# Kernel tuning notes

Hardware: AMD Instinct MI355X
Metric: run time of the kernel (lower is better)

Reference implementation:

```python
import jax, jax.numpy as jnp
import numpy as np

H = 16
D_MODEL = 1024
D_K = D_MODEL // H
SEQ = 2048
BATCH = 2


def setup_inputs() -> dict:
    key = jax.random.key(0)
    ks = jax.random.split(key, 11)
    s = 1.0 / np.sqrt(D_MODEL)
    inp = {
        "query": jax.random.normal(ks[0], (SEQ, BATCH, D_MODEL), jnp.float32),
        "key_": jax.random.normal(ks[1], (SEQ, BATCH, D_MODEL), jnp.float32),
        "value": jax.random.normal(ks[2], (SEQ, BATCH, D_MODEL), jnp.float32),
        "Wq": jax.random.uniform(ks[3], (D_MODEL, D_MODEL), jnp.float32, -s, s),
        "bq": jax.random.uniform(ks[4], (D_MODEL,), jnp.float32, -s, s),
        "Wk": jax.random.uniform(ks[5], (D_MODEL, D_MODEL), jnp.float32, -s, s),
        "bk": jax.random.uniform(ks[6], (D_MODEL,), jnp.float32, -s, s),
        "Wv": jax.random.uniform(ks[7], (D_MODEL, D_MODEL), jnp.float32, -s, s),
        "bv": jax.random.uniform(ks[8], (D_MODEL,), jnp.float32, -s, s),
        "Wo": jax.random.uniform(ks[9], (D_MODEL, D_MODEL), jnp.float32, -s, s),
        "bo": jax.random.uniform(ks[10], (D_MODEL,), jnp.float32, -s, s),
    }
    return inp


def _mha(query, key_, value, Wq, bq, Wk, bk, Wv, bv, Wo, bo):
    S, B, D = query.shape
    # torch Linear: x @ W.T + b; then view(S,B,h,dk).transpose(0,2) -> [h,B,S,dk]
    def proj(x, W, b):
        return jnp.transpose((x @ W.T + b).reshape(S, B, H, D_K), (2, 1, 0, 3))

    q = proj(query, Wq, bq)   # [h, b, S, dk]
    k = proj(key_, Wk, bk)
    v = proj(value, Wv, bv)

    scores = jnp.einsum("hbqd,hbkd->hbqk", q, k) / jnp.sqrt(
        jnp.asarray(D_K, q.dtype)
    )  # [h, b, S, S]
    p_attn = jax.nn.softmax(scores, axis=-1)  # dropout p=0.0 -> identity
    x = jnp.einsum("hbqk,hbkd->hbqd", p_attn, v)  # [h, b, S, dk]
    x = jnp.transpose(x, (2, 1, 0, 3)).reshape(S, B, D)  # back to [S, B, D]
    return x @ Wo.T + bo


def reference(query, key_, value, Wq, bq, Wk, bk, Wv, bv, Wo, bo):
    return _mha(query, key_, value, Wq, bq, Wk, bk, Wv, bv, Wo, bo)
```

## Files before the change

kernel.cpp:

```cpp
#include <hip/hip_runtime.h>

#define SEQ   2048
#define BATCH 2
#define DM    1024
#define NH    16
#define DKD   64
#define MROWS (SEQ*BATCH)

#define QSCALE 0.18033688011112042f

using bf16x8 = __attribute__((ext_vector_type(8))) __bf16;
using bf16x4 = __attribute__((ext_vector_type(4))) __bf16;
using bf16x2 = __attribute__((ext_vector_type(2))) __bf16;
using f32x4  = __attribute__((ext_vector_type(4))) float;
using f32x16 = __attribute__((ext_vector_type(16))) float;

__device__ __forceinline__ void gld_lds16(const __bf16* g, __bf16* l) {
  __builtin_amdgcn_global_load_lds(
      (__attribute__((address_space(1))) void*)(g),
      (__attribute__((address_space(3))) void*)(l), 16, 0, 0);
}

__global__ __launch_bounds__(256) void cvt_all(
    const float* __restrict__ s0, const float* __restrict__ s1,
    const float* __restrict__ s2, const float* __restrict__ s3,
    const float* __restrict__ s4, const float* __restrict__ s5,
    const float* __restrict__ s6,
    __bf16* __restrict__ d0, __bf16* __restrict__ d1, __bf16* __restrict__ d2,
    __bf16* __restrict__ d3, __bf16* __restrict__ d4, __bf16* __restrict__ d5,
    __bf16* __restrict__ d6, int n_big, int n_small) {
  int y = blockIdx.y;
  const float* s; __bf16* d;
  switch (y) {
    case 0: s = s0; d = d0; break;
    case 1: s = s1; d = d1; break;
    case 2: s = s2; d = d2; break;
    case 3: s = s3; d = d3; break;
    case 4: s = s4; d = d4; break;
    case 5: s = s5; d = d5; break;
    default: s = s6; d = d6; break;
  }
  int n = (y < 3) ? n_big : n_small;
  int i = (blockIdx.x * 256 + threadIdx.x) * 8;
  if (i >= n) return;
  const float4* sp = (const float4*)(s + i);
  float4 a = sp[0], b = sp[1];
  bf16x8 v;
  v[0]=(__bf16)a.x; v[1]=(__bf16)a.y; v[2]=(__bf16)a.z; v[3]=(__bf16)a.w;
  v[4]=(__bf16)b.x; v[5]=(__bf16)b.y; v[6]=(__bf16)b.z; v[7]=(__bf16)b.w;
  *(bf16x8*)(d + i) = v;
}

__device__ __forceinline__ void gemm_core(const __bf16* __restrict__ A,
                                          const __bf16* __restrict__ Bt,
                                          __bf16* Ash, __bf16* Bsh,
                                          f32x4 acc[4][4], int m0, int n0) {
  const int K = DM;
  int tid = threadIdx.x;
  int lane = tid & 63, quad = lane >> 4, l16 = lane & 15, sw = l16 & 7;
  int w = tid >> 6;
  int wm = (w & 1) * 64, wn = (w >> 1) * 64;
  for (int k0 = 0; k0 < K; k0 += 64) {
    __syncthreads();
#pragma unroll
    for (int it = 0; it < 4; ++it) {
      int c   = tid + it * 256;
      int row = c >> 3, pp = c & 7;
      int ko  = (pp ^ (row & 7)) << 3;
      int base = (tid - lane + it * 256) * 8;
      gld_lds16(A  + (size_t)(m0 + row) * K + k0 + ko, Ash + base);
      gld_lds16(Bt + (size_t)(n0 + row) * K + k0 + ko, Bsh + base);
    }
    __syncthreads();
#pragma unroll
    for (int kk = 0; kk < 2; ++kk) {
      bf16x8 af[4], bfr[4];
#pragma unroll
      for (int mi = 0; mi < 4; mi++)
        af[mi] = *(const bf16x8*)&Ash[(wm + mi * 16 + l16) * 64 +
                                      (((kk * 4 + quad) ^ sw) << 3)];
#pragma unroll
      for (int ni = 0; ni < 4; ni++)
        bfr[ni] = *(const bf16x8*)&Bsh[(wn + ni * 16 + l16) * 64 +
                                       (((kk * 4 + quad) ^ sw) << 3)];
#pragma unroll
      for (int mi = 0; mi < 4; mi++)
#pragma unroll
        for (int ni = 0; ni < 4; ni++)
          acc[mi][ni] = __builtin_amdgcn_mfma_f32_16x16x32_bf16(
              af[mi], bfr[ni], acc[mi][ni], 0, 0, 0);
    }
  }
}

__global__ __launch_bounds__(256, 3) void gemm_qkv(
    const __bf16* __restrict__ Xq, const __bf16* __restrict__ Xk,
    const __bf16* __restrict__ Xv, const __bf16* __restrict__ Wqkv,
    const float* __restrict__ bqp, const float* __restrict__ bkp,
    const float* __restrict__ bvp,
    __bf16* __restrict__ Qb, __bf16* __restrict__ Kb, __bf16* __restrict__ Vt) {
  __shared__ __bf16 Ash[128 * 64], Bsh[128 * 64];
  __shared__ __bf16 Esh[4][16 * 72];
  int z = blockIdx.z;
  const __bf16* A   = (z == 0) ? Xq : (z == 1) ? Xk : Xv;
  const __bf16* Bt  = Wqkv + (size_t)z * (DM * DM);
  const float* bias = (z == 0) ? bqp : (z == 1) ? bkp : bvp;
  int m0 = blockIdx.y * 128, n0 = blockIdx.x * 128;
  f32x4 acc[4][4] = {};
  gemm_core(A, Bt, Ash, Bsh, acc, m0, n0);

  int tid = threadIdx.x, lane = tid & 63, quad = lane >> 4, l16 = lane & 15;
  int w = tid >> 6, wm = (w & 1) * 64, wn = (w >> 1) * 64;
  __bf16* E = Esh[w];
  int n_base = n0 + wn;
  int hh = n_base >> 6;
  float scale = (z == 0) ? QSCALE : 1.0f;
  float bb[4];
#pragma unroll
  for (int ni = 0; ni < 4; ni++) bb[ni] = bias[n_base + ni * 16 + l16] * scale;

  if (z == 2) {
#pragma unroll
    for (int ni = 0; ni < 4; ni++) {
#pragma unroll
      for (int mi = 0; mi < 4; mi++) {
        int s0 = mi * 8 + quad * 2;
        bf16x2 p0, p1;
        p0[0] = (__bf16)(acc[mi][ni][0] + bb[ni]);
        p0[1] = (__bf16)(acc[mi][ni][2] + bb[ni]);
        p1[0] = (__bf16)(acc[mi][ni][1] + bb[ni]);
        p1[1] = (__bf16)(acc[mi][ni][3] + bb[ni]);
        *(bf16x2*)&E[l16 * 72 + s0]      = p0;
        *(bf16x2*)&E[l16 * 72 + 32 + s0] = p1;
      }
      asm volatile("s_waitcnt lgkmcnt(0)" ::: "memory");
#pragma unroll
      for (int pass = 0; pass < 2; pass++) {
        int ddl = pass * 8 + (lane >> 3);
        int col = (lane & 7) * 8;
        bf16x8 v = *(const bf16x8*)&E[ddl * 72 + col];
        int b2 = col >> 5, sl = col & 31;
        int dd = ni * 16 + ddl;
        int sg = ((m0 + wm) >> 1) + sl;
        *(bf16x8*)&Vt[(((size_t)hh * BATCH + b2) * DKD + dd) * SEQ + sg] = v;
      }
      asm volatile("s_waitcnt lgkmcnt(0)" ::: "memory");
    }
  } else {
    __bf16* Out = (z == 0) ? Qb : Kb;
#pragma unroll
    for (int mi = 0; mi < 4; mi++) {
#pragma unroll
      for (int ni = 0; ni < 4; ni++)
#pragma unroll
        for (int r = 0; r < 4; r++)
          E[(quad * 4 + r) * 72 + ni * 16 + l16] =
              (__bf16)fmaf(acc[mi][ni][r], scale, bb[ni]);
      asm volatile("s_waitcnt lgkmcnt(0)" ::: "memory");
#pragma unroll
      for (int pass = 0; pass < 2; pass++) {
        int row16 = pass * 8 + (lane >> 3);
        int coll  = (lane & 7) * 8;
        bf16x8 v = *(const bf16x8*)&E[row16 * 72 + coll];
        int m = m0 + wm + mi * 16 + row16;
        int s = m >> 1, b2 = m & 1;
        *(bf16x8*)&Out[(((size_t)hh * BATCH + b2) * SEQ + s) * DKD + coll] = v;
      }
      asm volatile("s_waitcnt lgkmcnt(0)" ::: "memory");
    }
  }
}

__global__ __launch_bounds__(256, 3) void gemm_out(
    const __bf16* __restrict__ A, const __bf16* __restrict__ Bt,
    const float* __restrict__ bias, float* __restrict__ out) {
  __shared__ __bf16 Ash[64 * 64], Bsh[128 * 64];
  const int K = DM;
  int m0 = blockIdx.y * 64, n0 = blockIdx.x * 128;
  int tid = threadIdx.x;
  int lane = tid & 63, quad = lane >> 4, l16 = lane & 15, sw = l16 & 7;
  int w = tid >> 6;
  int wm = (w & 1) * 32, wn = (w >> 1) * 64;
  f32x4 acc[2][4] = {};
  for (int k0 = 0; k0 < K; k0 += 64) {
    __syncthreads();
#pragma unroll
    for (int it = 0; it < 2; ++it) {
      int c = tid + it * 256;
      int row = c >> 3, pp = c & 7;
      int ko = (pp ^ (row & 7)) << 3;
      gld_lds16(A + (size_t)(m0 + row) * K + k0 + ko,
                Ash + (tid - lane + it * 256) * 8);
    }
#pragma unroll
    for (int it = 0; it < 4; ++it) {
      int c = tid + it * 256;
      int row = c >> 3, pp = c & 7;
      int ko = (pp ^ (row & 7)) << 3;
      gld_lds16(Bt + (size_t)(n0 + row) * K + k0 + ko,
                Bsh + (tid - lane + it * 256) * 8);
    }
    __syncthreads();
#pragma unroll
    for (int kk = 0; kk < 2; ++kk) {
      bf16x8 af[2], bfr[4];
#pragma unroll
      for (int mi = 0; mi < 2; mi++)
        af[mi] = *(const bf16x8*)&Ash[(wm + mi * 16 + l16) * 64 +
                                      (((kk * 4 + quad) ^ sw) << 3)];
#pragma unroll
      for (int ni = 0; ni < 4; ni++)
        bfr[ni] = *(const bf16x8*)&Bsh[(wn + ni * 16 + l16) * 64 +
                                       (((kk * 4 + quad) ^ sw) << 3)];
#pragma unroll
      for (int mi = 0; mi < 2; mi++)
#pragma unroll
        for (int ni = 0; ni < 4; ni++)
          acc[mi][ni] = __builtin_amdgcn_mfma_f32_16x16x32_bf16(
              af[mi], bfr[ni], acc[mi][ni], 0, 0, 0);
    }
  }
#pragma unroll
  for (int ni = 0; ni < 4; ni++) {
    int n = n0 + wn + ni * 16 + l16;
    float bb = bias[n];
#pragma unroll
    for (int mi = 0; mi < 2; mi++) {
#pragma unroll
      for (int r = 0; r < 4; r++) {
        int m = m0 + wm + mi * 16 + quad * 4 + r;
        out[(size_t)m * DM + n] = acc[mi][ni][r] + bb;
      }
    }
  }
}

__global__ __launch_bounds__(256, 2) void flash_attn(
    const __bf16* __restrict__ Qg, const __bf16* __restrict__ Kg,
    const __bf16* __restrict__ Vtg, __bf16* __restrict__ Xa) {
  __shared__ __bf16 Ksh[2][64 * 64];
  __shared__ __bf16 Vsh[2][64 * 64];
  int tid = threadIdx.x, w = tid >> 6, lane = tid & 63;
  int l32 = lane & 31, hf = lane >> 5;
  int n = blockIdx.x;
  int hb = n & 31, qi = n >> 5;
  int hd = hb >> 1, b = hb & 1, q0 = qi * 128;
  int qbase = q0 + w * 32;
  size_t hboff = ((size_t)hd * BATCH + b) * SEQ * DKD;
  const __bf16* Qp = Qg + hboff;
  const __bf16* Kp = Kg + hboff;
  const __bf16* Vp = Vtg + hboff;

  bf16x8 qf[4];
#pragma unroll
  for (int kd = 0; kd < 4; kd++)
    qf[kd] = *(const bf16x8*)(
        Qp + (size_t)(qbase + l32) * DKD + kd * 16 + hf * 8);

  f32x16 o0 = {0,0,0,0,0,0,0,0,0,0,0,0,0,0,0,0};
  f32x16 o1 = {0,0,0,0,0,0,0,0,0,0,0,0,0,0,0,0};
  float l0 = 0.f, l1 = 0.f;

#pragma unroll
  for (int it = 0; it < 2; ++it) {
    int c = tid + it * 256;
    int r = c >> 3, pp = c & 7;
    int off = (pp ^ (r & 7)) << 3;
    gld_lds16(Kp + (size_t)r * DKD + off, Ksh[0] + c * 8);
    gld_lds16(Vp + (size_t)r * SEQ + off, Vsh[0] + c * 8);
  }

  for (int t = 0; t < SEQ / 64; ++t) {
    __syncthreads();
    if (t + 1 < SEQ / 64) {
      int k0n = (t + 1) * 64, bn = (t + 1) & 1;
#pragma unroll
      for (int it = 0; it < 2; ++it) {
        int c = tid + it * 256;
        int r = c >> 3, pp = c & 7;
        int off = (pp ^ (r & 7)) << 3;
        gld_lds16(Kp + (size_t)(k0n + r) * DKD + off, Ksh[bn] + c * 8);
        gld_lds16(Vp + (size_t)r * SEQ + k0n + off, Vsh[bn] + c * 8);
      }
    }
    const __bf16* Kb_ = Ksh[t & 1];
    const __bf16* Vb_ = Vsh[t & 1];

#pragma unroll
    for (int jt = 0; jt < 2; ++jt) {
      int rk = jt * 32 + l32;
      f32x16 s = {0,0,0,0,0,0,0,0,0,0,0,0,0,0,0,0};
#pragma unroll
      for (int kd = 0; kd < 4; kd++) {
        bf16x8 kf = *(const bf16x8*)&Kb_[rk * 64 +
                                         (((kd * 2 + hf) ^ (rk & 7)) << 3)];
        s = __builtin_amdgcn_mfma_f32_32x32x16_bf16(kf, qf[kd], s, 0, 0, 0);
      }
      unsigned L[4][2];
#pragma unroll
      for (int bq = 0; bq < 4; bq++) {
        float p0 = exp2f(s[4 * bq + 0]);
        float p1 = exp2f(s[4 * bq + 1]);
        float p2 = exp2f(s[4 * bq + 2]);
        float p3 = exp2f(s[4 * bq + 3]);
        l0 += p0 + p2;
        l1 += p1 + p3;
        asm("v_cvt_pk_bf16_f32 %0, %1, %2" : "=v"(L[bq][0]) : "v"(p0), "v"(p1));
        asm("v_cvt_pk_bf16_f32 %0, %1, %2" : "=v"(L[bq][1]) : "v"(p2), "v"(p3));
      }
#pragma unroll
      for (int kp = 0; kp < 2; kp++) {
        unsigned a0 = L[2 * kp][0], b0 = L[2 * kp + 1][0];
        unsigned a1 = L[2 * kp][1], b1 = L[2 * kp + 1][1];
        asm("v_permlane32_swap_b32 %0, %1" : "+v"(a0), "+v"(b0));
        asm("v_permlane32_swap_b32 %0, %1" : "+v"(a1), "+v"(b1));
        unsigned pw[4] = {a0, a1, b0, b1};
        bf16x8 pa;
        __builtin_memcpy(&pa, pw, 16);
        int ks = jt * 2 + kp;
        {
          int rv = l32;
          bf16x8 vb = *(const bf16x8*)&Vb_[rv * 64 +
                                           (((ks * 2 + hf) ^ (rv & 7)) << 3)];
          o0 = __builtin_amdgcn_mfma_f32_32x32x16_bf16(pa, vb, o0, 0, 0, 0);
        }
        {
          int rv = 32 + l32;
          bf16x8 vb = *(const bf16x8*)&Vb_[rv * 64 +
                                           (((ks * 2 + hf) ^ (rv & 7)) << 3)];
          o1 = __builtin_amdgcn_mfma_f32_32x32x16_bf16(pa, vb, o1, 0, 0, 0);
        }
      }
    }
  }

  float l_ = l0 + l1;
  l_ += __shfl_xor(l_, 32, 64);
  float linv = 1.0f / l_;

#pragma unroll
  for (int r = 0; r < 16; ++r) {
    int qrow = (r & 3) + 8 * (r >> 2) + 4 * hf;
    float li = __shfl(linv, qrow, 64);
    int q = qbase + qrow;
    __bf16* dst = Xa + ((size_t)q * BATCH + b) * DM + hd * DKD;
    dst[l32]      = (__bf16)(o0[r] * li);
    dst[32 + l32] = (__bf16)(o1[r] * li);
  }
}

extern "C" void kernel_launch(void* const* d_in, const int* in_sizes, int n_in,
                              void* d_out, int out_size, void* d_ws,
                              size_t ws_size, hipStream_t stream) {
  (void)in_sizes; (void)n_in; (void)out_size; (void)ws_size;
  const float* query = (const float*)d_in[0];
  const float* key_  = (const float*)d_in[1];
  const float* value = (const float*)d_in[2];
  const float* Wq = (const float*)d_in[3];
  const float* bq = (const float*)d_in[4];
  const float* Wk = (const float*)d_in[5];
  const float* bk = (const float*)d_in[6];
  const float* Wv = (const float*)d_in[7];
  const float* bv = (const float*)d_in[8];
  const float* Wo = (const float*)d_in[9];
  const float* bo = (const float*)d_in[10];

  const size_t NX = (size_t)MROWS * DM;
  const size_t NW = (size_t)DM * DM;
  __bf16* p    = (__bf16*)d_ws;
  __bf16* Xq   = p; p += NX;
  __bf16* Xk   = p; p += NX;
  __bf16* Xv   = p; p += NX;
  __bf16* Wqkv = p; p += 3 * NW;
  __bf16* Wob  = p; p += NW;
  __bf16* Qb   = p; p += NX;
  __bf16* Kb   = p; p += NX;
  __bf16* Vt   = p; p += NX;
  __bf16* Xa   = Xq;

  cvt_all<<<dim3((unsigned)(NX / 2048), 7), 256, 0, stream>>>(
      query, key_, value, Wq, Wk, Wv, Wo,
      Xq, Xk, Xv, Wqkv, Wqkv + NW, Wqkv + 2 * NW, Wob, (int)NX, (int)NW);

  gemm_qkv<<<dim3(DM / 128, MROWS / 128, 3), 256, 0, stream>>>(
      Xq, Xk, Xv, Wqkv, bq, bk, bv, Qb, Kb, Vt);
  flash_attn<<<dim3(512), 256, 0, stream>>>(Qb, Kb, Vt, Xa);
  gemm_out<<<dim3(DM / 128, MROWS / 64), 256, 0, stream>>>(
      Xa, Wob, bo, (float*)d_out);
}
```

Baseline: 225.9 us.

## Split attention over key halves with fp32 partials and a combine kernel

Each attention block now processes half of the key sequence, doubling the grid to fill more compute units, and launch bounds are raised to allow more blocks per CU. Unnormalized fp32 partial outputs and row sums are written to workspace, and a new combine kernel sums them, normalizes, and converts to bf16. This relies on the fixed-scale softmax having no running max, so the partials add directly. The trade-off is extra global memory traffic for the fp32 partials and an additional kernel launch.

```diff
diff --git a/kernel.cpp b/kernel.cpp
--- a/kernel.cpp
+++ b/kernel.cpp
@@ -235,17 +235,22 @@
   }
 }
 
-__global__ __launch_bounds__(256, 2) void flash_attn(
+__global__ __launch_bounds__(256, 4) void flash_attn(
     const __bf16* __restrict__ Qg, const __bf16* __restrict__ Kg,
-    const __bf16* __restrict__ Vtg, __bf16* __restrict__ Xa) {
+    const __bf16* __restrict__ Vtg,
+    float* __restrict__ Op0, float* __restrict__ Op1,
+    float* __restrict__ Lp0, float* __restrict__ Lp1) {
   __shared__ __bf16 Ksh[2][64 * 64];
   __shared__ __bf16 Vsh[2][64 * 64];
   int tid = threadIdx.x, w = tid >> 6, lane = tid & 63;
   int l32 = lane & 31, hf = lane >> 5;
   int n = blockIdx.x;
-  int hb = n & 31, qi = n >> 5;
+  int hb = n & 31, qi = (n >> 5) & 15, jh = n >> 9;
   int hd = hb >> 1, b = hb & 1, q0 = qi * 128;
   int qbase = q0 + w * 32;
+  int t0 = jh * 16;
+  float* Op = jh ? Op1 : Op0;
+  float* Lp = jh ? Lp1 : Lp0;
   size_t hboff = ((size_t)hd * BATCH + b) * SEQ * DKD;
   const __bf16* Qp = Qg + hboff;
   const __bf16* Kp = Kg + hboff;
@@ -266,14 +271,14 @@
     int c = tid + it * 256;
     int r = c >> 3, pp = c & 7;
     int off = (pp ^ (r & 7)) << 3;
-    gld_lds16(Kp + (size_t)r * DKD + off, Ksh[0] + c * 8);
-    gld_lds16(Vp + (size_t)r * SEQ + off, Vsh[0] + c * 8);
-  }
-
-  for (int t = 0; t < SEQ / 64; ++t) {
+    gld_lds16(Kp + (size_t)(t0 * 64 + r) * DKD + off, Ksh[0] + c * 8);
+    gld_lds16(Vp + (size_t)r * SEQ + t0 * 64 + off, Vsh[0] + c * 8);
+  }
+
+  for (int tt = 0; tt < 16; ++tt) {
     __syncthreads();
-    if (t + 1 < SEQ / 64) {
-      int k0n = (t + 1) * 64, bn = (t + 1) & 1;
+    if (tt + 1 < 16) {
+      int k0n = (t0 + tt + 1) * 64, bn = (tt + 1) & 1;
 #pragma unroll
       for (int it = 0; it < 2; ++it) {
         int c = tid + it * 256;
@@ -283,8 +288,8 @@
         gld_lds16(Vp + (size_t)r * SEQ + k0n + off, Vsh[bn] + c * 8);
       }
     }
-    const __bf16* Kb_ = Ksh[t & 1];
-    const __bf16* Vb_ = Vsh[t & 1];
+    const __bf16* Kb_ = Ksh[tt & 1];
+    const __bf16* Vb_ = Vsh[tt & 1];
 
 #pragma unroll
     for (int jt = 0; jt < 2; ++jt) {
@@ -336,17 +341,41 @@
 
   float l_ = l0 + l1;
   l_ += __shfl_xor(l_, 32, 64);
-  float linv = 1.0f / l_;
+  if (hf == 0)
+    Lp[((size_t)hd * BATCH + b) * SEQ + qbase + l32] = l_;
 
 #pragma unroll
   for (int r = 0; r < 16; ++r) {
     int qrow = (r & 3) + 8 * (r >> 2) + 4 * hf;
-    float li = __shfl(linv, qrow, 64);
     int q = qbase + qrow;
-    __bf16* dst = Xa + ((size_t)q * BATCH + b) * DM + hd * DKD;
-    dst[l32]      = (__bf16)(o0[r] * li);
-    dst[32 + l32] = (__bf16)(o1[r] * li);
-  }
+    float* dst = Op + ((size_t)q * BATCH + b) * DM + hd * DKD;
+    dst[l32]      = o0[r];
+    dst[32 + l32] = o1[r];
+  }
+}
+
+__global__ __launch_bounds__(256) void attn_combine(
+    const float* __restrict__ Op0, const float* __restrict__ Op1,
+    const float* __restrict__ Lp0, const float* __restrict__ Lp1,
+    __bf16* __restrict__ Xa) {
+  int i = (blockIdx.x * 256 + threadIdx.x) * 8;
+  int row = i >> 10, col = i & 1023;
+  int q = row >> 1, b = row & 1, h = col >> 6;
+  size_t li = ((size_t)h * BATCH + b) * SEQ + q;
+  float linv = 1.0f / (Lp0[li] + Lp1[li]);
+  const float4* a = (const float4*)(Op0 + i);
+  const float4* c = (const float4*)(Op1 + i);
+  float4 a0 = a[0], a1 = a[1], c0 = c[0], c1 = c[1];
+  bf16x8 v;
+  v[0] = (__bf16)((a0.x + c0.x) * linv);
+  v[1] = (__bf16)((a0.y + c0.y) * linv);
+  v[2] = (__bf16)((a0.z + c0.z) * linv);
+  v[3] = (__bf16)((a0.w + c0.w) * linv);
+  v[4] = (__bf16)((a1.x + c1.x) * linv);
+  v[5] = (__bf16)((a1.y + c1.y) * linv);
+  v[6] = (__bf16)((a1.z + c1.z) * linv);
+  v[7] = (__bf16)((a1.w + c1.w) * linv);
+  *(bf16x8*)(Xa + i) = v;
 }
 
 extern "C" void kernel_launch(void* const* d_in, const int* in_sizes, int n_in,
@@ -367,6 +396,7 @@
 
   const size_t NX = (size_t)MROWS * DM;
   const size_t NW = (size_t)DM * DM;
+  const size_t NL = (size_t)NH * BATCH * SEQ;
   __bf16* p    = (__bf16*)d_ws;
   __bf16* Xq   = p; p += NX;
   __bf16* Xk   = p; p += NX;
@@ -376,6 +406,10 @@
   __bf16* Qb   = p; p += NX;
   __bf16* Kb   = p; p += NX;
   __bf16* Vt   = p; p += NX;
+  float*  Op1  = (float*)p; p += 2 * NX;
+  float*  Lp0  = (float*)p; p += 2 * NL;
+  float*  Lp1  = (float*)p; p += 2 * NL;
+  float*  Op0  = (float*)Xk;
   __bf16* Xa   = Xq;
 
   cvt_all<<<dim3((unsigned)(NX / 2048), 7), 256, 0, stream>>>(
@@ -384,7 +418,9 @@
 
   gemm_qkv<<<dim3(DM / 128, MROWS / 128, 3), 256, 0, stream>>>(
       Xq, Xk, Xv, Wqkv, bq, bk, bv, Qb, Kb, Vt);
-  flash_attn<<<dim3(512), 256, 0, stream>>>(Qb, Kb, Vt, Xa);
+  flash_attn<<<dim3(1024), 256, 0, stream>>>(Qb, Kb, Vt, Op0, Op1, Lp0, Lp1);
+  attn_combine<<<dim3((unsigned)(NX / 2048)), 256, 0, stream>>>(
+      Op0, Op1, Lp0, Lp1, Xa);
   gemm_out<<<dim3(DM / 128, MROWS / 64), 256, 0, stream>>>(
       Xa, Wob, bo, (float*)d_out);
 }
```

New measurement: 235.8 us. 4.4% more time.

## Fuse activation fp32-to-bf16 conversion into QKV GEMM loads and retile output GEMM

Applied to the files above, without the earlier changes.

The query/key/value conversion is moved out of the standalone conversion kernel and done inside the QKV GEMM's A-tile load path: fp32 is read, converted in registers, and stored to LDS. This removes the write and re-read of three bf16 activation buffers, and the conversion kernel now handles only the weights. The output GEMM switches to 128x128 tiles using the shared core, and both GEMM grids swap their x/y axes so the M tiles vary fastest. The trade-off is that A is now loaded synchronously through registers instead of via async global-to-LDS loads, and it is read at twice the byte volume, once per N tile.

```diff
diff --git a/kernel.cpp b/kernel.cpp
--- a/kernel.cpp
+++ b/kernel.cpp
@@ -21,28 +21,21 @@
       (__attribute__((address_space(3))) void*)(l), 16, 0, 0);
 }
 
-__global__ __launch_bounds__(256) void cvt_all(
+__global__ __launch_bounds__(256) void cvt_w(
     const float* __restrict__ s0, const float* __restrict__ s1,
     const float* __restrict__ s2, const float* __restrict__ s3,
-    const float* __restrict__ s4, const float* __restrict__ s5,
-    const float* __restrict__ s6,
     __bf16* __restrict__ d0, __bf16* __restrict__ d1, __bf16* __restrict__ d2,
-    __bf16* __restrict__ d3, __bf16* __restrict__ d4, __bf16* __restrict__ d5,
-    __bf16* __restrict__ d6, int n_big, int n_small) {
-  int y = blockIdx.y;
+    __bf16* __restrict__ d3) {
+  int c = blockIdx.x * 256 + threadIdx.x;
+  int y = c >> 17;
+  long i = (long)(c & 0x1FFFF) * 8;
   const float* s; __bf16* d;
   switch (y) {
     case 0: s = s0; d = d0; break;
     case 1: s = s1; d = d1; break;
     case 2: s = s2; d = d2; break;
-    case 3: s = s3; d = d3; break;
-    case 4: s = s4; d = d4; break;
-    case 5: s = s5; d = d5; break;
-    default: s = s6; d = d6; break;
-  }
-  int n = (y < 3) ? n_big : n_small;
-  int i = (blockIdx.x * 256 + threadIdx.x) * 8;
-  if (i >= n) return;
+    default: s = s3; d = d3; break;
+  }
   const float4* sp = (const float4*)(s + i);
   float4 a = sp[0], b = sp[1];
   bf16x8 v;
@@ -93,21 +86,74 @@
   }
 }
 
+__device__ __forceinline__ void gemm_core_f32a(const float* __restrict__ Af,
+                                               const __bf16* __restrict__ Bt,
+                                               __bf16* Ash, __bf16* Bsh,
+                                               f32x4 acc[4][4], int m0, int n0) {
+  const int K = DM;
+  int tid = threadIdx.x;
+  int lane = tid & 63, quad = lane >> 4, l16 = lane & 15, sw = l16 & 7;
+  int w = tid >> 6;
+  int wm = (w & 1) * 64, wn = (w >> 1) * 64;
+  for (int k0 = 0; k0 < K; k0 += 64) {
+    __syncthreads();
+#pragma unroll
+    for (int it = 0; it < 4; ++it) {
+      int c   = tid + it * 256;
+      int row = c >> 3, pp = c & 7;
+      int ko  = (pp ^ (row & 7)) << 3;
+      gld_lds16(Bt + (size_t)(n0 + row) * K + k0 + ko,
+                Bsh + (tid - lane + it * 256) * 8);
+    }
+#pragma unroll
+    for (int it = 0; it < 4; ++it) {
+      int c   = tid + it * 256;
+      int row = c >> 3, pp = c & 7;
+      int ko  = (pp ^ (row & 7)) << 3;
+      const float4* sp = (const float4*)(Af + (size_t)(m0 + row) * K + k0 + ko);
+      float4 a = sp[0], b = sp[1];
+      bf16x8 v;
+      v[0]=(__bf16)a.x; v[1]=(__bf16)a.y; v[2]=(__bf16)a.z; v[3]=(__bf16)a.w;
+      v[4]=(__bf16)b.x; v[5]=(__bf16)b.y; v[6]=(__bf16)b.z; v[7]=(__bf16)b.w;
+      *(bf16x8*)(Ash + c * 8) = v;
+    }
+    __syncthreads();
+#pragma unroll
+    for (int kk = 0; kk < 2; ++kk) {
+      bf16x8 af[4], bfr[4];
+#pragma unroll
+      for (int mi = 0; mi < 4; mi++)
+        af[mi] = *(const bf16x8*)&Ash[(wm + mi * 16 + l16) * 64 +
+                                      (((kk * 4 + quad) ^ sw) << 3)];
+#pragma unroll
+      for (int ni = 0; ni < 4; ni++)
+        bfr[ni] = *(const bf16x8*)&Bsh[(wn + ni * 16 + l16) * 64 +
+                                       (((kk * 4 + quad) ^ sw) << 3)];
+#pragma unroll
+      for (int mi = 0; mi < 4; mi++)
+#pragma unroll
+        for (int ni = 0; ni < 4; ni++)
+          acc[mi][ni] = __builtin_amdgcn_mfma_f32_16x16x32_bf16(
+              af[mi], bfr[ni], acc[mi][ni], 0, 0, 0);
+    }
+  }
+}
+
 __global__ __launch_bounds__(256, 3) void gemm_qkv(
-    const __bf16* __restrict__ Xq, const __bf16* __restrict__ Xk,
-    const __bf16* __restrict__ Xv, const __bf16* __restrict__ Wqkv,
+    const float* __restrict__ Xq, const float* __restrict__ Xk,
+    const float* __restrict__ Xv, const __bf16* __restrict__ Wqkv,
     const float* __restrict__ bqp, const float* __restrict__ bkp,
     const float* __restrict__ bvp,
     __bf16* __restrict__ Qb, __bf16* __restrict__ Kb, __bf16* __restrict__ Vt) {
   __shared__ __bf16 Ash[128 * 64], Bsh[128 * 64];
   __shared__ __bf16 Esh[4][16 * 72];
   int z = blockIdx.z;
-  const __bf16* A   = (z == 0) ? Xq : (z == 1) ? Xk : Xv;
+  const float* A    = (z == 0) ? Xq : (z == 1) ? Xk : Xv;
   const __bf16* Bt  = Wqkv + (size_t)z * (DM * DM);
   const float* bias = (z == 0) ? bqp : (z == 1) ? bkp : bvp;
-  int m0 = blockIdx.y * 128, n0 = blockIdx.x * 128;
+  int m0 = blockIdx.x * 128, n0 = blockIdx.y * 128;
   f32x4 acc[4][4] = {};
-  gemm_core(A, Bt, Ash, Bsh, acc, m0, n0);
+  gemm_core_f32a(A, Bt, Ash, Bsh, acc, m0, n0);
 
   int tid = threadIdx.x, lane = tid & 63, quad = lane >> 4, l16 = lane & 15;
   int w = tid >> 6, wm = (w & 1) * 64, wn = (w >> 1) * 64;
@@ -174,58 +220,21 @@
 __global__ __launch_bounds__(256, 3) void gemm_out(
     const __bf16* __restrict__ A, const __bf16* __restrict__ Bt,
     const float* __restrict__ bias, float* __restrict__ out) {
-  __shared__ __bf16 Ash[64 * 64], Bsh[128 * 64];
-  const int K = DM;
-  int m0 = blockIdx.y * 64, n0 = blockIdx.x * 128;
+  __shared__ __bf16 Ash[128 * 64], Bsh[128 * 64];
+  int m0 = blockIdx.x * 128, n0 = blockIdx.y * 128;
+  f32x4 acc[4][4] = {};
+  gemm_core(A, Bt, Ash, Bsh, acc, m0, n0);
+
   int tid = threadIdx.x;
-  int lane = tid & 63, quad = lane >> 4, l16 = lane & 15, sw = l16 & 7;
+  int lane = tid & 63, quad = lane >> 4, l16 = lane & 15;
   int w = tid >> 6;
-  int wm = (w & 1) * 32, wn = (w >> 1) * 64;
-  f32x4 acc[2][4] = {};
-  for (int k0 = 0; k0 < K; k0 += 64) {
-    __syncthreads();
-#pragma unroll
-    for (int it = 0; it < 2; ++it) {
-      int c = tid + it * 256;
-      int row = c >> 3, pp = c & 7;
-      int ko = (pp ^ (row & 7)) << 3;
-      gld_lds16(A + (size_t)(m0 + row) * K + k0 + ko,
-                Ash + (tid - lane + it * 256) * 8);
-    }
-#pragma unroll
-    for (int it = 0; it < 4; ++it) {
-      int c = tid + it * 256;
-      int row = c >> 3, pp = c & 7;
-      int ko = (pp ^ (row & 7)) << 3;
-      gld_lds16(Bt + (size_t)(n0 + row) * K + k0 + ko,
-                Bsh + (tid - lane + it * 256) * 8);
-    }
-    __syncthreads();
-#pragma unroll
-    for (int kk = 0; kk < 2; ++kk) {
-      bf16x8 af[2], bfr[4];
-#pragma unroll
-      for (int mi = 0; mi < 2; mi++)
-        af[mi] = *(const bf16x8*)&Ash[(wm + mi * 16 + l16) * 64 +
-                                      (((kk * 4 + quad) ^ sw) << 3)];
-#pragma unroll
-      for (int ni = 0; ni < 4; ni++)
-        bfr[ni] = *(const bf16x8*)&Bsh[(wn + ni * 16 + l16) * 64 +
-                                       (((kk * 4 + quad) ^ sw) << 3)];
-#pragma unroll
-      for (int mi = 0; mi < 2; mi++)
-#pragma unroll
-        for (int ni = 0; ni < 4; ni++)
-          acc[mi][ni] = __builtin_amdgcn_mfma_f32_16x16x32_bf16(
-              af[mi], bfr[ni], acc[mi][ni], 0, 0, 0);
-    }
-  }
+  int wm = (w & 1) * 64, wn = (w >> 1) * 64;
 #pragma unroll
   for (int ni = 0; ni < 4; ni++) {
     int n = n0 + wn + ni * 16 + l16;
     float bb = bias[n];
 #pragma unroll
-    for (int mi = 0; mi < 2; mi++) {
+    for (int mi = 0; mi < 4; mi++) {
 #pragma unroll
       for (int r = 0; r < 4; r++) {
         int m = m0 + wm + mi * 16 + quad * 4 + r;
@@ -244,7 +253,8 @@
   int l32 = lane & 31, hf = lane >> 5;
   int n = blockIdx.x;
   int hb = n & 31, qi = n >> 5;
-  int hd = hb >> 1, b = hb & 1, q0 = qi * 128;
+  int hd = hb >> 1, b = hb & 1;
+  int q0 = qi * 128;
   int qbase = q0 + w * 32;
   size_t hboff = ((size_t)hd * BATCH + b) * SEQ * DKD;
   const __bf16* Qp = Qg + hboff;
@@ -368,23 +378,19 @@
   const size_t NX = (size_t)MROWS * DM;
   const size_t NW = (size_t)DM * DM;
   __bf16* p    = (__bf16*)d_ws;
-  __bf16* Xq   = p; p += NX;
-  __bf16* Xk   = p; p += NX;
-  __bf16* Xv   = p; p += NX;
+  __bf16* Xa   = p; p += NX;
   __bf16* Wqkv = p; p += 3 * NW;
   __bf16* Wob  = p; p += NW;
   __bf16* Qb   = p; p += NX;
   __bf16* Kb   = p; p += NX;
   __bf16* Vt   = p; p += NX;
-  __bf16* Xa   = Xq;
-
-  cvt_all<<<dim3((unsigned)(NX / 2048), 7), 256, 0, stream>>>(
-      query, key_, value, Wq, Wk, Wv, Wo,
-      Xq, Xk, Xv, Wqkv, Wqkv + NW, Wqkv + 2 * NW, Wob, (int)NX, (int)NW);
-
-  gemm_qkv<<<dim3(DM / 128, MROWS / 128, 3), 256, 0, stream>>>(
-      Xq, Xk, Xv, Wqkv, bq, bk, bv, Qb, Kb, Vt);
+
+  cvt_w<<<dim3(2048), 256, 0, stream>>>(
+      Wq, Wk, Wv, Wo, Wqkv, Wqkv + NW, Wqkv + 2 * NW, Wob);
+
+  gemm_qkv<<<dim3(MROWS / 128, DM / 128, 3), 256, 0, stream>>>(
+      query, key_, value, Wqkv, bq, bk, bv, Qb, Kb, Vt);
   flash_attn<<<dim3(512), 256, 0, stream>>>(Qb, Kb, Vt, Xa);
-  gemm_out<<<dim3(DM / 128, MROWS / 64), 256, 0, stream>>>(
+  gemm_out<<<dim3(MROWS / 128, DM / 128), 256, 0, stream>>>(
       Xa, Wob, bo, (float*)d_out);
 }
```

Result: no change. 229.0 us (+1.4%).
